# Performance work log

Hardware: AMD Instinct MI355X
Metric: run time of the kernel (lower is better)

## Reference

```python
import jax, jax.numpy as jnp
import numpy as np

B, S, H = 32, 4096, 1024


def setup_inputs() -> dict:
    key = jax.random.key(0)
    k1, k2 = jax.random.split(key)
    lstm_outputs = jax.random.normal(k1, (B, S, H), dtype=jnp.float32)
    w_attn = jax.random.normal(k2, (H,), dtype=jnp.float32) * (1.0 / np.sqrt(H))
    return {"lstm_outputs": lstm_outputs, "w_attn": w_attn}


def reference(lstm_outputs, w_attn):
    # energy: [B, S] = tanh(lstm_outputs @ w)
    energy = jnp.tanh(jnp.einsum("bsh,h->bs", lstm_outputs, w_attn))
    attn = jax.nn.softmax(energy, axis=1)  # softmax over sequence dim
    # context: [B, H] weighted sum over sequence
    context = jnp.einsum("bs,bsh->bh", attn, lstm_outputs)
    return context
```

## Files before the change

### kernel.cpp

```cpp
#include <hip/hip_runtime.h>
#include <math.h>

#define BB 32
#define SS 4096
#define HH 1024
#define CHUNKS 16
#define ROWS_PER_BLOCK (SS / CHUNKS)
#define WAVES 4
#define ROWS_PER_WAVE (ROWS_PER_BLOCK / WAVES)
#define UNROLL 4

__global__ __launch_bounds__(256, 2) void attn_pass1(
    const float* __restrict__ x, const float* __restrict__ w,
    float* __restrict__ pc, float* __restrict__ pl)
{
    const int tid  = threadIdx.x;
    const int wave = tid >> 6;
    const int lane = tid & 63;
    const int blk  = blockIdx.x;
    const int b    = blk / CHUNKS;
    const int chunk= blk % CHUNKS;

    const float* xb = x + (long long)b * SS * HH
                        + (long long)chunk * ROWS_PER_BLOCK * HH
                        + (long long)wave * ROWS_PER_WAVE * HH;

    float4 wv[4];
#pragma unroll
    for (int k = 0; k < 4; ++k)
        wv[k] = *(const float4*)(w + k * 256 + lane * 4);

    float4 acc[4];
#pragma unroll
    for (int k = 0; k < 4; ++k) acc[k] = make_float4(0.f, 0.f, 0.f, 0.f);
    float l = 0.f;

    for (int r = 0; r < ROWS_PER_WAVE; r += UNROLL) {
        float4 xv[UNROLL][4];
        const float* p = xb + (long long)r * HH + lane * 4;
#pragma unroll
        for (int u = 0; u < UNROLL; ++u)
#pragma unroll
            for (int k = 0; k < 4; ++k)
                xv[u][k] = *(const float4*)(p + u * HH + k * 256);

        float s[UNROLL];
#pragma unroll
        for (int u = 0; u < UNROLL; ++u) {
            float t = 0.f;
#pragma unroll
            for (int k = 0; k < 4; ++k) {
                t = fmaf(xv[u][k].x, wv[k].x, t);
                t = fmaf(xv[u][k].y, wv[k].y, t);
                t = fmaf(xv[u][k].z, wv[k].z, t);
                t = fmaf(xv[u][k].w, wv[k].w, t);
            }
            s[u] = t;
        }
#pragma unroll
        for (int off = 32; off >= 1; off >>= 1)
#pragma unroll
            for (int u = 0; u < UNROLL; ++u)
                s[u] += __shfl_xor(s[u], off, 64);

#pragma unroll
        for (int u = 0; u < UNROLL; ++u) {
            float pw = __expf(tanhf(s[u]));
            l += pw;
#pragma unroll
            for (int k = 0; k < 4; ++k) {
                acc[k].x = fmaf(pw, xv[u][k].x, acc[k].x);
                acc[k].y = fmaf(pw, xv[u][k].y, acc[k].y);
                acc[k].z = fmaf(pw, xv[u][k].z, acc[k].z);
                acc[k].w = fmaf(pw, xv[u][k].w, acc[k].w);
            }
        }
    }

    __shared__ float lds_c[WAVES * HH];
    __shared__ float lds_l[WAVES];
#pragma unroll
    for (int k = 0; k < 4; ++k)
        *(float4*)(lds_c + wave * HH + k * 256 + lane * 4) = acc[k];
    if (lane == 0) lds_l[wave] = l;
    __syncthreads();

    float4 c = *(const float4*)(lds_c + tid * 4);
#pragma unroll
    for (int wv2 = 1; wv2 < WAVES; ++wv2) {
        float4 o = *(const float4*)(lds_c + wv2 * HH + tid * 4);
        c.x += o.x; c.y += o.y; c.z += o.z; c.w += o.w;
    }
    *(float4*)(pc + (long long)blk * HH + tid * 4) = c;
    if (tid == 0)
        pl[blk] = lds_l[0] + lds_l[1] + lds_l[2] + lds_l[3];
}

__global__ __launch_bounds__(256) void attn_pass2(
    const float* __restrict__ pc, const float* __restrict__ pl,
    float* __restrict__ out)
{
    const int b = blockIdx.x;
    const int t = threadIdx.x;
    float l = 0.f;
    float4 c = make_float4(0.f, 0.f, 0.f, 0.f);
#pragma unroll
    for (int i = 0; i < CHUNKS; ++i) {
        const int blk = b * CHUNKS + i;
        l += pl[blk];
        float4 o = *(const float4*)(pc + (long long)blk * HH + t * 4);
        c.x += o.x; c.y += o.y; c.z += o.z; c.w += o.w;
    }
    const float inv = 1.f / l;
    float4 r = make_float4(c.x * inv, c.y * inv, c.z * inv, c.w * inv);
    *(float4*)(out + (long long)b * HH + t * 4) = r;
}

extern "C" void kernel_launch(void* const* d_in, const int* in_sizes, int n_in,
                              void* d_out, int out_size, void* d_ws, size_t ws_size,
                              hipStream_t stream) {
    const float* x = (const float*)d_in[0];
    const float* w = (const float*)d_in[1];
    float* out = (float*)d_out;

    float* pc = (float*)d_ws;
    float* pl = pc + (size_t)BB * CHUNKS * HH;

    attn_pass1<<<BB * CHUNKS, 256, 0, stream>>>(x, w, pc, pl);
    attn_pass2<<<BB, 256, 0, stream>>>(pc, pl, out);
}
```

Before: 677.8 us.

## Double-buffer row loads in attention pass1 and use fast tanh approximation

Pass 1 now uses register double-buffering, so loads of the next pair of rows are issued before the current pair is processed. This hides global memory latency in a kernel bound by memory bandwidth. The chunk count doubles to give more blocks, UNROLL drops to 2, and the launch-bounds occupancy hint rises to 3. tanhf is replaced with an exp/rcp formulation, which trades a little accuracy for fewer instructions; that formula can overflow to inf for large inputs, but the rcp result is still handled correctly.

```diff
diff --git a/kernel.cpp b/kernel.cpp
--- a/kernel.cpp
+++ b/kernel.cpp
@@ -4,13 +4,64 @@
 #define BB 32
 #define SS 4096
 #define HH 1024
-#define CHUNKS 16
+#define CHUNKS 32
 #define ROWS_PER_BLOCK (SS / CHUNKS)
 #define WAVES 4
 #define ROWS_PER_WAVE (ROWS_PER_BLOCK / WAVES)
-#define UNROLL 4
+#define UNROLL 2
 
-__global__ __launch_bounds__(256, 2) void attn_pass1(
+__device__ __forceinline__ float softmax_w(float s) {
+    float t  = __expf(2.0f * s);
+    float th = 1.0f - 2.0f * __builtin_amdgcn_rcpf(t + 1.0f);
+    return __expf(th);
+}
+
+__device__ __forceinline__ void load_rows(float4 (&buf)[UNROLL][4],
+                                          const float* __restrict__ p) {
+#pragma unroll
+    for (int u = 0; u < UNROLL; ++u)
+#pragma unroll
+        for (int k = 0; k < 4; ++k)
+            buf[u][k] = *(const float4*)(p + u * HH + k * 256);
+}
+
+__device__ __forceinline__ void process_rows(const float4 (&buf)[UNROLL][4],
+                                             const float4 (&wv)[4],
+                                             float4 (&acc)[4], float& l) {
+    float s[UNROLL];
+#pragma unroll
+    for (int u = 0; u < UNROLL; ++u) {
+        float t = 0.f;
+#pragma unroll
+        for (int k = 0; k < 4; ++k) {
+            t = fmaf(buf[u][k].x, wv[k].x, t);
+            t = fmaf(buf[u][k].y, wv[k].y, t);
+            t = fmaf(buf[u][k].z, wv[k].z, t);
+            t = fmaf(buf[u][k].w, wv[k].w, t);
+        }
+        s[u] = t;
+    }
+#pragma unroll
+    for (int off = 32; off >= 1; off >>= 1)
+#pragma unroll
+        for (int u = 0; u < UNROLL; ++u)
+            s[u] += __shfl_xor(s[u], off, 64);
+
+#pragma unroll
+    for (int u = 0; u < UNROLL; ++u) {
+        float pw = softmax_w(s[u]);
+        l += pw;
+#pragma unroll
+        for (int k = 0; k < 4; ++k) {
+            acc[k].x = fmaf(pw, buf[u][k].x, acc[k].x);
+            acc[k].y = fmaf(pw, buf[u][k].y, acc[k].y);
+            acc[k].z = fmaf(pw, buf[u][k].z, acc[k].z);
+            acc[k].w = fmaf(pw, buf[u][k].w, acc[k].w);
+        }
+    }
+}
+
+__global__ __launch_bounds__(256, 3) void attn_pass1(
     const float* __restrict__ x, const float* __restrict__ w,
     float* __restrict__ pc, float* __restrict__ pl)
 {
@@ -23,7 +74,8 @@
 
     const float* xb = x + (long long)b * SS * HH
                         + (long long)chunk * ROWS_PER_BLOCK * HH
-                        + (long long)wave * ROWS_PER_WAVE * HH;
+                        + (long long)wave * ROWS_PER_WAVE * HH
+                        + lane * 4;
 
     float4 wv[4];
 #pragma unroll
@@ -35,46 +87,15 @@
     for (int k = 0; k < 4; ++k) acc[k] = make_float4(0.f, 0.f, 0.f, 0.f);
     float l = 0.f;
 
-    for (int r = 0; r < ROWS_PER_WAVE; r += UNROLL) {
-        float4 xv[UNROLL][4];
-        const float* p = xb + (long long)r * HH + lane * 4;
-#pragma unroll
-        for (int u = 0; u < UNROLL; ++u)
-#pragma unroll
-            for (int k = 0; k < 4; ++k)
-                xv[u][k] = *(const float4*)(p + u * HH + k * 256);
+    float4 bufA[UNROLL][4], bufB[UNROLL][4];
+    load_rows(bufA, xb);
 
-        float s[UNROLL];
-#pragma unroll
-        for (int u = 0; u < UNROLL; ++u) {
-            float t = 0.f;
-#pragma unroll
-            for (int k = 0; k < 4; ++k) {
-                t = fmaf(xv[u][k].x, wv[k].x, t);
-                t = fmaf(xv[u][k].y, wv[k].y, t);
-                t = fmaf(xv[u][k].z, wv[k].z, t);
-                t = fmaf(xv[u][k].w, wv[k].w, t);
-            }
-            s[u] = t;
-        }
-#pragma unroll
-        for (int off = 32; off >= 1; off >>= 1)
-#pragma unroll
-            for (int u = 0; u < UNROLL; ++u)
-                s[u] += __shfl_xor(s[u], off, 64);
-
-#pragma unroll
-        for (int u = 0; u < UNROLL; ++u) {
-            float pw = __expf(tanhf(s[u]));
-            l += pw;
-#pragma unroll
-            for (int k = 0; k < 4; ++k) {
-                acc[k].x = fmaf(pw, xv[u][k].x, acc[k].x);
-                acc[k].y = fmaf(pw, xv[u][k].y, acc[k].y);
-                acc[k].z = fmaf(pw, xv[u][k].z, acc[k].z);
-                acc[k].w = fmaf(pw, xv[u][k].w, acc[k].w);
-            }
-        }
+    for (int r = 0; r < ROWS_PER_WAVE; r += 2 * UNROLL) {
+        load_rows(bufB, xb + (long long)(r + UNROLL) * HH);
+        process_rows(bufA, wv, acc, l);
+        if (r + 2 * UNROLL < ROWS_PER_WAVE)
+            load_rows(bufA, xb + (long long)(r + 2 * UNROLL) * HH);
+        process_rows(bufB, wv, acc, l);
     }
 
     __shared__ float lds_c[WAVES * HH];
```

Result: no change. 676.4 us (-0.2%).

## Double-buffer input rows into LDS via async global_load_lds and use fast tanh

Applied to the files above, without the earlier changes.

Replaces the direct register loads of input rows with asynchronous global-to-LDS transfers (global_load_lds) into a per-wave double buffer, so the next two-row tile is in flight while the current tile is processed. This aims to keep more memory requests outstanding and hide latency in the bandwidth-bound pass. It also replaces tanhf with an exp/rcp formulation, which is cheaper but slightly less accurate. The LDS footprint grows to 64KB per block, which may limit occupancy, and the manual vmcnt waits depend on the exact instruction count.

```diff
diff --git a/kernel.cpp b/kernel.cpp
--- a/kernel.cpp
+++ b/kernel.cpp
@@ -1,5 +1,6 @@
 #include <hip/hip_runtime.h>
 #include <math.h>
+#include <stdint.h>
 
 #define BB 32
 #define SS 4096
@@ -8,12 +9,33 @@
 #define ROWS_PER_BLOCK (SS / CHUNKS)
 #define WAVES 4
 #define ROWS_PER_WAVE (ROWS_PER_BLOCK / WAVES)
-#define UNROLL 4
+#define TROWS 2
+#define NTILES (ROWS_PER_WAVE / TROWS)
+
+typedef __attribute__((address_space(3))) uint32_t lds_u32_t;
+typedef const __attribute__((address_space(1))) uint32_t glb_u32_t;
+
+__device__ __forceinline__ void stage_tile(const float* gsrc, float* ldst) {
+#pragma unroll
+    for (int seg = 0; seg < 8; ++seg) {
+        __builtin_amdgcn_global_load_lds(
+            (glb_u32_t*)(gsrc + seg * 256),
+            (lds_u32_t*)(ldst + seg * 256), 16, 0, 0);
+    }
+}
+
+__device__ __forceinline__ float softmax_w(float s) {
+    float t  = __expf(2.0f * s);
+    float th = 1.0f - 2.0f * __builtin_amdgcn_rcpf(t + 1.0f);
+    return __expf(th);
+}
 
 __global__ __launch_bounds__(256, 2) void attn_pass1(
     const float* __restrict__ x, const float* __restrict__ w,
     float* __restrict__ pc, float* __restrict__ pl)
 {
+    __shared__ float lds[2][WAVES][TROWS * HH];
+
     const int tid  = threadIdx.x;
     const int wave = tid >> 6;
     const int lane = tid & 63;
@@ -21,9 +43,12 @@
     const int b    = blk / CHUNKS;
     const int chunk= blk % CHUNKS;
 
-    const float* xb = x + (long long)b * SS * HH
+    const float* xw = x + (long long)b * SS * HH
                         + (long long)chunk * ROWS_PER_BLOCK * HH
                         + (long long)wave * ROWS_PER_WAVE * HH;
+    const float* gsrc = xw + lane * 4;
+
+    stage_tile(gsrc, &lds[0][wave][0]);
 
     float4 wv[4];
 #pragma unroll
@@ -35,37 +60,46 @@
     for (int k = 0; k < 4; ++k) acc[k] = make_float4(0.f, 0.f, 0.f, 0.f);
     float l = 0.f;
 
-    for (int r = 0; r < ROWS_PER_WAVE; r += UNROLL) {
-        float4 xv[UNROLL][4];
-        const float* p = xb + (long long)r * HH + lane * 4;
+    for (int t = 0; t < NTILES; ++t) {
+        const int cur = t & 1;
+        if (t + 1 < NTILES) {
+            stage_tile(gsrc + (long long)(t + 1) * TROWS * HH,
+                       &lds[1 - cur][wave][0]);
+            asm volatile("s_waitcnt vmcnt(8)" ::: "memory");
+        } else {
+            asm volatile("s_waitcnt vmcnt(0)" ::: "memory");
+        }
+
+        const float* lp = &lds[cur][wave][0] + lane * 4;
+        float4 xv[TROWS][4];
 #pragma unroll
-        for (int u = 0; u < UNROLL; ++u)
+        for (int u = 0; u < TROWS; ++u)
 #pragma unroll
             for (int k = 0; k < 4; ++k)
-                xv[u][k] = *(const float4*)(p + u * HH + k * 256);
+                xv[u][k] = *(const float4*)(lp + u * HH + k * 256);
 
-        float s[UNROLL];
+        float s[TROWS];
 #pragma unroll
-        for (int u = 0; u < UNROLL; ++u) {
-            float t = 0.f;
+        for (int u = 0; u < TROWS; ++u) {
+            float tacc = 0.f;
 #pragma unroll
             for (int k = 0; k < 4; ++k) {
-                t = fmaf(xv[u][k].x, wv[k].x, t);
-                t = fmaf(xv[u][k].y, wv[k].y, t);
-                t = fmaf(xv[u][k].z, wv[k].z, t);
-                t = fmaf(xv[u][k].w, wv[k].w, t);
+                tacc = fmaf(xv[u][k].x, wv[k].x, tacc);
+                tacc = fmaf(xv[u][k].y, wv[k].y, tacc);
+                tacc = fmaf(xv[u][k].z, wv[k].z, tacc);
+                tacc = fmaf(xv[u][k].w, wv[k].w, tacc);
             }
-            s[u] = t;
+            s[u] = tacc;
         }
 #pragma unroll
         for (int off = 32; off >= 1; off >>= 1)
 #pragma unroll
-            for (int u = 0; u < UNROLL; ++u)
+            for (int u = 0; u < TROWS; ++u)
                 s[u] += __shfl_xor(s[u], off, 64);
 
 #pragma unroll
-        for (int u = 0; u < UNROLL; ++u) {
-            float pw = __expf(tanhf(s[u]));
+        for (int u = 0; u < TROWS; ++u) {
+            float pw = softmax_w(s[u]);
             l += pw;
 #pragma unroll
             for (int k = 0; k < 4; ++k) {
@@ -77,23 +111,24 @@
         }
     }
 
-    __shared__ float lds_c[WAVES * HH];
-    __shared__ float lds_l[WAVES];
+    __syncthreads();
+    float* red  = &lds[0][0][0];
+    float* redl = &lds[1][0][0];
 #pragma unroll
     for (int k = 0; k < 4; ++k)
-        *(float4*)(lds_c + wave * HH + k * 256 + lane * 4) = acc[k];
-    if (lane == 0) lds_l[wave] = l;
+        *(float4*)(red + wave * HH + k * 256 + lane * 4) = acc[k];
+    if (lane == 0) redl[wave] = l;
     __syncthreads();
 
-    float4 c = *(const float4*)(lds_c + tid * 4);
+    float4 c = *(const float4*)(red + tid * 4);
 #pragma unroll
     for (int wv2 = 1; wv2 < WAVES; ++wv2) {
-        float4 o = *(const float4*)(lds_c + wv2 * HH + tid * 4);
+        float4 o = *(const float4*)(red + wv2 * HH + tid * 4);
         c.x += o.x; c.y += o.y; c.z += o.z; c.w += o.w;
     }
     *(float4*)(pc + (long long)blk * HH + tid * 4) = c;
     if (tid == 0)
-        pl[blk] = lds_l[0] + lds_l[1] + lds_l[2] + lds_l[3];
+        pl[blk] = redl[0] + redl[1] + redl[2] + redl[3];
 }
 
 __global__ __launch_bounds__(256) void attn_pass2(
```

Result: no change. 681.2 us (+0.5%).
